# Performance work log

Hardware: AMD Instinct MI355X
Metric: run time of the kernel (lower is better)

Reference implementation:

```python
import jax, jax.numpy as jnp
import numpy as np

B, S, HN, TN = 8, 32, 64, 512
HID, EMB, VOCAB = 512, 512, 10000


def setup_inputs():
    key = jax.random.key(0)
    k = jax.random.split(key, 14)
    w = lambda kk, shape: jax.random.normal(kk, shape, jnp.float32) * 0.02
    return {
        "dec_out": jax.random.normal(k[0], (B, S, HID), jnp.float32),
        "history": jax.random.normal(k[1], (B, HID), jnp.float32),
        "head": jax.random.randint(k[2], (B, HN), 0, VOCAB),
        "tail": jax.random.randint(k[3], (B, TN), 0, VOCAB),
        "adj_mask": jax.random.randint(k[4], (B, HN, TN), 0, 2).astype(bool),
        "dup_mask": jax.random.randint(k[5], (B, S, TN), 0, 2).astype(bool),
        "emb_table": w(k[6], (VOCAB, EMB)),
        "W_tq": w(k[7], (2 * HID + EMB, HID)),
        "b_tq": jnp.zeros((HID,), jnp.float32),
        "W_tk": w(k[8], (EMB, HID)),
        "b_tk": jnp.zeros((HID,), jnp.float32),
        "W_tout": w(k[9], (2 * HID, HID)),
        "W_hq": w(k[10], (2 * HID, HID)),
        "b_hq": jnp.zeros((HID,), jnp.float32),
        "W_hk": w(k[11], (HID, HID)),
        "b_hk": jnp.zeros((HID,), jnp.float32),
    }


def reference(dec_out, history, head, tail, adj_mask, dup_mask, emb_table,
              W_tq, b_tq, W_tk, b_tk, W_tout, W_hq, b_hq, W_hk, b_hk):
    head_emb = emb_table[head]  # (B, HN, EMB)
    tail_emb = emb_table[tail]  # (B, TN, EMB)

    # --- tail attention query: Linear(cat([dec_out, history, head_emb])) + ELU.
    # Same math as the torch broadcast-concat, computed as a sum of three
    # partial matmuls to avoid materializing the (B,S,HN,2*hid+emb) concat.
    Wd, Wh, We = W_tq[:HID], W_tq[HID:2 * HID], W_tq[2 * HID:]
    tq = jax.nn.elu((dec_out @ Wd)[:, :, None, :]
                    + (history @ Wh)[:, None, None, :]
                    + (head_emb @ We)[:, None, :, :]
                    + b_tq)                       # (B, S, HN, HID)
    tq = tq.reshape(B, S * HN, HID)
    tk = jax.nn.elu(tail_emb @ W_tk + b_tk)       # (B, TN, HID)  (dropout=eval)

    # combined logical mask: allowed = adjacency AND not-duplicate
    mask = (adj_mask[:, None, :, :] & ~dup_mask[:, :, None, :]).reshape(B, S * HN, TN)

    # GlobalAttention (dot): score -> mask -> softmax -> context -> tanh(linear_out([c;q]))
    scores = jnp.einsum('bqh,bth->bqt', tq, tk)   # (B, S*HN, TN)
    tail_attn = jax.nn.softmax(jnp.where(mask, scores, -jnp.inf), axis=-1)
    ctx = jnp.einsum('bqt,bth->bqh', tail_attn, tk)
    graph_hid = jnp.tanh(ctx @ W_tout[:HID] + tq @ W_tout[HID:])
    graph_hid = graph_hid.reshape(B * S, HN, HID)
    tail_attn = tail_attn.reshape(B * S, HN, TN)

    # --- head attention (one-step), length-masked over HN
    hq = jax.nn.elu(dec_out @ W_hq[:HID] + (history @ W_hq[HID:])[:, None, :] + b_hq)
    hq = hq.reshape(B * S, HID)
    hk = jax.nn.elu(jnp.einsum('nkh,hd->nkd', graph_hid, W_hk) + b_hk)
    lengths = jnp.repeat(jnp.sum(head != 0, axis=-1), S)          # (B*S,)
    hscores = jnp.einsum('nh,nkh->nk', hq, hk)                    # (B*S, HN)
    lmask = jnp.arange(HN)[None, :] < lengths[:, None]
    head_attn = jax.nn.softmax(jnp.where(lmask, hscores, -jnp.inf), axis=-1)
    # (head-attention context output is discarded by the original module)

    prob = jnp.einsum('nk,nkt->nt', head_attn, tail_attn).reshape(B, S, TN)
    return jnp.log(prob + 1e-20)
```

## Files before the change

kernel.cpp:

```cpp
#include <hip/hip_runtime.h>
#include <math.h>

#define BB 8
#define SS 32
#define HN 64
#define TN 512
#define HID 512

typedef __attribute__((ext_vector_type(8))) short short8;
typedef __attribute__((ext_vector_type(4))) float f32x4;

__device__ __forceinline__ float eluf(float x) { return x > 0.f ? x : (expf(x) - 1.f); }

__device__ __forceinline__ short f2bs(float f) {
    union { float f; unsigned int u; } v; v.f = f;
    unsigned int r = v.u + 0x7fffu + ((v.u >> 16) & 1u);
    return (short)(r >> 16);
}
__device__ __forceinline__ float b2f(short s) {
    union { unsigned int u; float f; } v;
    v.u = ((unsigned int)(unsigned short)s) << 16;
    return v.f;
}

__device__ __forceinline__ void gld16(const void* g, void* l) {
    __builtin_amdgcn_global_load_lds(
        (const __attribute__((address_space(1))) void*)g,
        (__attribute__((address_space(3))) void*)l, 16, 0, 0);
}

template <int ACT, int OUTB>
__device__ __forceinline__ void gcore(
    const short* __restrict__ A, const short* __restrict__ B,
    const float* __restrict__ bias, void* __restrict__ Cv,
    int ldc, int K, int m0, int n0, int cm0, short* Ls)
{
    short* Al = Ls;
    short* Bl = Ls + 8192;
    const int tid  = threadIdx.x;
    const int lane = tid & 63;
    const int w    = tid >> 6;
    const int wr   = w >> 1, wc = w & 1;
    const int l16  = lane & 15, quad = lane >> 4;

    const int srow = w * 16 + (lane >> 2);
    const int scol = (lane & 3) * 8;

    f32x4 acc[4][4];
#pragma unroll
    for (int i = 0; i < 4; ++i)
#pragma unroll
        for (int j = 0; j < 4; ++j) { acc[i][j][0]=0.f; acc[i][j][1]=0.f; acc[i][j][2]=0.f; acc[i][j][3]=0.f; }

    short* lA = Al + w * 512;
    short* lB = Bl + w * 512;
    const long rstep = (long)64 * K;

    const short* Ag = A + (long)(m0 + srow) * K + scol;
    const short* Bg = B + (long)(n0 + srow) * K + scol;
    for (int kt = 0; kt < K; kt += 64) {
        __syncthreads();
        gld16(Ag + kt, lA);
        gld16(Ag + kt + rstep, lA + 2048);
        gld16(Ag + kt + 32, lA + 4096);
        gld16(Ag + kt + 32 + rstep, lA + 4096 + 2048);
        gld16(Bg + kt, lB);
        gld16(Bg + kt + rstep, lB + 2048);
        gld16(Bg + kt + 32, lB + 4096);
        gld16(Bg + kt + 32 + rstep, lB + 4096 + 2048);
        __syncthreads();
#pragma unroll
        for (int h = 0; h < 2; ++h) {
            short8 af[4], bf4[4];
#pragma unroll
            for (int mi = 0; mi < 4; ++mi)
                af[mi] = *(const short8*)(Al + h * 4096 + (wr * 64 + mi * 16 + l16) * 32 + quad * 8);
#pragma unroll
            for (int ni = 0; ni < 4; ++ni)
                bf4[ni] = *(const short8*)(Bl + h * 4096 + (wc * 64 + ni * 16 + l16) * 32 + quad * 8);
#pragma unroll
            for (int mi = 0; mi < 4; ++mi)
#pragma unroll
                for (int ni = 0; ni < 4; ++ni)
                    acc[mi][ni] = __builtin_amdgcn_mfma_f32_16x16x32_bf16(af[mi], bf4[ni], acc[mi][ni], 0, 0, 0);
        }
    }

    __syncthreads();

    float bv[4];
#pragma unroll
    for (int ni = 0; ni < 4; ++ni)
        bv[ni] = bias ? bias[n0 + wc * 64 + ni * 16 + l16] : 0.f;

    if (OUTB == 1) {
        short* eb = Ls + w * 1152;
        const int er = lane >> 2;
        const int ec = (lane & 3) * 16;
#pragma unroll
        for (int mi = 0; mi < 4; ++mi) {
#pragma unroll
            for (int ni = 0; ni < 4; ++ni)
#pragma unroll
                for (int r = 0; r < 4; ++r) {
                    float x = acc[mi][ni][r] + bv[ni];
                    if (ACT == 1) x = eluf(x);
                    eb[(quad * 4 + r) * 72 + ni * 16 + l16] = f2bs(x);
                }
            __builtin_amdgcn_sched_barrier(0);
            short8 v0 = *(const short8*)&eb[er * 72 + ec];
            short8 v1 = *(const short8*)&eb[er * 72 + ec + 8];
            long cb = (long)(cm0 + wr * 64 + mi * 16 + er) * ldc + n0 + wc * 64 + ec;
            *(short8*)((short*)Cv + cb)     = v0;
            *(short8*)((short*)Cv + cb + 8) = v1;
            __builtin_amdgcn_sched_barrier(0);
        }
    } else {
#pragma unroll
        for (int mi = 0; mi < 4; ++mi)
#pragma unroll
            for (int ni = 0; ni < 4; ++ni) {
                int gc = n0 + wc * 64 + ni * 16 + l16;
#pragma unroll
                for (int r = 0; r < 4; ++r) {
                    float x = acc[mi][ni][r] + bv[ni];
                    if (ACT == 1) x = eluf(x);
                    ((float*)Cv)[(long)(cm0 + wr * 64 + mi * 16 + quad * 4 + r) * ldc + gc] = x;
                }
            }
    }
}

template <int ACT, int OUTB, int DUAL>
__device__ __forceinline__ void gcoreB(
    const short* __restrict__ A, const short* __restrict__ B,
    const short* __restrict__ A2, const short* __restrict__ B2,
    const float* __restrict__ bias, void* __restrict__ Cv,
    int ldc, int K, int m0, int n0, int cm0, short* Ls,
    const float* __restrict__ hq, float* __restrict__ hsp)
{
    short* Al = Ls;
    short* Bl = Ls + 16384;
    const int tid  = threadIdx.x;
    const int lane = tid & 63;
    const int w    = tid >> 6;
    const int wr   = w >> 1, wc = w & 1;
    const int l16  = lane & 15, quad = lane >> 4;

    const int srow = w * 16 + (lane >> 2);
    const int scol = (lane & 3) * 8;

    f32x4 acc[4][4];
#pragma unroll
    for (int i = 0; i < 4; ++i)
#pragma unroll
        for (int j = 0; j < 4; ++j) { acc[i][j][0]=0.f; acc[i][j][1]=0.f; acc[i][j][2]=0.f; acc[i][j][3]=0.f; }

    short* lA = Al + w * 512;
    short* lB = Bl + w * 512;
    const long rstep = (long)64 * K;

    for (int rep = 0; rep <= DUAL; ++rep) {
        const short* Ag = (rep ? A2 : A) + (long)(m0 + srow) * K + scol;
        const short* Bg = (rep ? B2 : B) + (long)(n0 + srow) * K + scol;
        for (int kt = 0; kt < K; kt += 128) {
            __syncthreads();
#pragma unroll
            for (int h = 0; h < 4; ++h) {
                gld16(Ag + kt + h * 32,         lA + h * 4096);
                gld16(Ag + kt + h * 32 + rstep, lA + h * 4096 + 2048);
                gld16(Bg + kt + h * 32,         lB + h * 4096);
                gld16(Bg + kt + h * 32 + rstep, lB + h * 4096 + 2048);
            }
            __syncthreads();
#pragma unroll
            for (int h = 0; h < 4; ++h) {
                short8 af[4], bf4[4];
#pragma unroll
                for (int mi = 0; mi < 4; ++mi)
                    af[mi] = *(const short8*)(Al + h * 4096 + (wr * 64 + mi * 16 + l16) * 32 + quad * 8);
#pragma unroll
                for (int ni = 0; ni < 4; ++ni)
                    bf4[ni] = *(const short8*)(Bl + h * 4096 + (wc * 64 + ni * 16 + l16) * 32 + quad * 8);
#pragma unroll
                for (int mi = 0; mi < 4; ++mi)
#pragma unroll
                    for (int ni = 0; ni < 4; ++ni)
                        acc[mi][ni] = __builtin_amdgcn_mfma_f32_16x16x32_bf16(af[mi], bf4[ni], acc[mi][ni], 0, 0, 0);
            }
        }
    }

    __syncthreads();

    float bv[4];
#pragma unroll
    for (int ni = 0; ni < 4; ++ni)
        bv[ni] = bias ? bias[n0 + wc * 64 + ni * 16 + l16] : 0.f;

    if (OUTB == 1) {
        short* eb = Ls + w * 1152;
        const int er = lane >> 2;
        const int ec = (lane & 3) * 16;
#pragma unroll
        for (int mi = 0; mi < 4; ++mi) {
#pragma unroll
            for (int ni = 0; ni < 4; ++ni)
#pragma unroll
                for (int r = 0; r < 4; ++r) {
                    float x = acc[mi][ni][r] + bv[ni];
                    if (ACT == 1) x = eluf(x);
                    else if (ACT == 2) x = tanhf(x);
                    eb[(quad * 4 + r) * 72 + ni * 16 + l16] = f2bs(x);
                }
            __builtin_amdgcn_sched_barrier(0);
            short8 v0 = *(const short8*)&eb[er * 72 + ec];
            short8 v1 = *(const short8*)&eb[er * 72 + ec + 8];
            long cb = (long)(cm0 + wr * 64 + mi * 16 + er) * ldc + n0 + wc * 64 + ec;
            *(short8*)((short*)Cv + cb)     = v0;
            *(short8*)((short*)Cv + cb + 8) = v1;
            __builtin_amdgcn_sched_barrier(0);
        }
    } else if (OUTB == 2) {
        const int n_w = (cm0 + wr * 64) >> 6;
        float hqv[4];
#pragma unroll
        for (int ni = 0; ni < 4; ++ni)
            hqv[ni] = hq[(long)n_w * 512 + n0 + wc * 64 + ni * 16 + l16];
        float* red = (float*)Ls;
#pragma unroll
        for (int mi = 0; mi < 4; ++mi)
#pragma unroll
            for (int r = 0; r < 4; ++r) {
                float p = 0.f;
#pragma unroll
                for (int ni = 0; ni < 4; ++ni) {
                    float x = acc[mi][ni][r] + bv[ni];
                    if (ACT == 1) x = eluf(x);
                    p += x * hqv[ni];
                }
                p += __shfl_xor(p, 1);
                p += __shfl_xor(p, 2);
                p += __shfl_xor(p, 4);
                p += __shfl_xor(p, 8);
                if (l16 == 0) red[w * 64 + mi * 16 + quad * 4 + r] = p;
            }
        __syncthreads();
        if (tid < 128) {
            int wr2 = tid >> 6, rw = tid & 63;
            float v = red[(wr2 * 2 + 0) * 64 + rw] + red[(wr2 * 2 + 1) * 64 + rw];
            hsp[(long)(n0 >> 7) * 16384 + cm0 + tid] = v;
        }
    }
}

template <int ACT, int OUTB, int DUAL, int NYL2>
__global__ __launch_bounds__(256) void mgemm_sw(
    const short* __restrict__ A, long sAz,
    const short* __restrict__ B, long sBz,
    const short* __restrict__ A2, long sA2z,
    const short* __restrict__ B2,
    const float* __restrict__ bias,
    void* __restrict__ Cv, long sCz, int ldc, int K)
{
    __shared__ short Ls[32768];
    const int bid = blockIdx.x;
    const int g = (bid & 7) + 8 * (bid >> 5);
    const int x = (bid >> 3) & 3;
    const int y = g & ((1 << NYL2) - 1);
    const int z = g >> NYL2;
    void* C = (void*)((short*)Cv + (long)z * sCz);
    const short* A2z = DUAL ? (A2 + (long)z * sA2z) : nullptr;
    gcoreB<ACT, OUTB, DUAL>(A + (long)z * sAz, B + (long)z * sBz, A2z, B2, bias, C,
                            ldc, K, y * 128, x * 128, y * 128, Ls, nullptr, nullptr);
}

__global__ __launch_bounds__(256) void mgemm_hs(
    const short* __restrict__ A, const short* __restrict__ B,
    const float* __restrict__ bias, const float* __restrict__ hq, float* __restrict__ hsp)
{
    __shared__ short Ls[32768];
    const int bid = blockIdx.x;
    const int y = (bid & 7) + 8 * (bid >> 5);
    const int x = (bid >> 3) & 3;
    gcoreB<1, 2, 0>(A, B, nullptr, nullptr, bias, nullptr, 512, 512,
                    y * 128, x * 128, y * 128, Ls, hq, hsp);
}

__global__ __launch_bounds__(256) void mgemm_multi(
    const short* __restrict__ decb, const short* __restrict__ WTall, float* __restrict__ qall,
    const short* __restrict__ embAll, const short* __restrict__ WTe, float* __restrict__ qe,
    const short* __restrict__ WTk, const float* __restrict__ b_tk, short* __restrict__ tkb)
{
    __shared__ short Ls[16384];
    int id = blockIdx.x;
    if (id < 48) {
        int y = id >> 4, x = id & 15;
        gcore<0, 0>(decb, WTall, nullptr, qall, 2048, 512, y * 128, x * 128, y * 128, Ls);
    } else if (id < 64) {
        int id2 = id - 48, y = id2 >> 2, x = id2 & 3;
        gcore<0, 0>(embAll, WTe, nullptr, qe, 512, 512, y * 128, x * 128, y * 128, Ls);
    } else {
        int id3 = id - 64, y = id3 >> 2, x = id3 & 3;
        gcore<1, 1>(embAll, WTk, b_tk, tkb, 512, 512, 512 + y * 128, x * 128, y * 128, Ls);
    }
}

struct WTDesc { const float* src[9]; short* dst[9]; };

__global__ __launch_bounds__(256) void prep(
    const float* __restrict__ dec_out, const float* __restrict__ history,
    short* __restrict__ decb,
    const float* __restrict__ emb, const int* __restrict__ head, const int* __restrict__ tail,
    short* __restrict__ embAll, WTDesc wd)
{
    __shared__ float t[32][33];
    const int id = blockIdx.x, tid = threadIdx.x;
    if (id < 132) {
        int i = (id * 256 + tid) * 4;
        float4 v = (i < 131072) ? *(const float4*)(dec_out + i)
                                : *(const float4*)(history + (i - 131072));
        short4 o;
        o.x = f2bs(v.x); o.y = f2bs(v.y); o.z = f2bs(v.z); o.w = f2bs(v.w);
        *(short4*)(decb + i) = o;
    } else if (id < 132 + 2304) {
        int r = (id - 132) * 2 + (tid >> 7);
        int c4 = (tid & 127) * 4;
        int idx = (r < 512) ? head[r] : tail[r - 512];
        float4 v = *(const float4*)(emb + (long)idx * 512 + c4);
        short4 o;
        o.x = f2bs(v.x); o.y = f2bs(v.y); o.z = f2bs(v.z); o.w = f2bs(v.w);
        *(short4*)(embAll + (long)r * 512 + c4) = o;
    } else {
        int q = id - 2436;
        int z = q >> 8, xy = q & 255;
        int x = xy & 15, y = xy >> 4;
        const float* src = wd.src[z];
        short* dst = wd.dst[z];
        int k0 = y * 32, n0 = x * 32;
        int tx = tid & 31, ty = tid >> 5;
#pragma unroll
        for (int i = 0; i < 32; i += 8)
            t[ty + i][tx] = src[(long)(k0 + ty + i) * 512 + n0 + tx];
        __syncthreads();
#pragma unroll
        for (int i = 0; i < 32; i += 8)
            dst[(long)(n0 + ty + i) * 512 + k0 + tx] = f2bs(t[tx][ty + i]);
    }
}

__global__ __launch_bounds__(256) void l3_kernel(
    const float* __restrict__ qall, const float* __restrict__ qe,
    const float* __restrict__ b_tq, short* __restrict__ tqb,
    const short* __restrict__ WTo1, const short* __restrict__ tkb, short* __restrict__ tkWTb,
    const float* __restrict__ b_hq, float* __restrict__ hqf)
{
    __shared__ short Ls[16384];
    if (blockIdx.x < 8192) {
        long gid = (long)blockIdx.x * 256 + threadIdx.x;
        int r = (int)(gid >> 7), j0 = ((int)gid & 127) * 4;
        int b = r >> 11, rem = r & 2047, s = rem >> 6, h = rem & 63;
        float4 d = *(const float4*)(qall + (long)(b * 32 + s) * 2048 + j0);
        float4 q = *(const float4*)(qall + (long)(256 + b) * 2048 + 1024 + j0);
        float4 e = *(const float4*)(qe + (long)(b * 64 + h) * 512 + j0);
        float4 bb = *(const float4*)(b_tq + j0);
        short4 o;
        o.x = f2bs(eluf(d.x + q.x + e.x + bb.x));
        o.y = f2bs(eluf(d.y + q.y + e.y + bb.y));
        o.z = f2bs(eluf(d.z + q.z + e.z + bb.z));
        o.w = f2bs(eluf(d.w + q.w + e.w + bb.w));
        *(short4*)(tqb + (long)r * 512 + j0) = o;
    } else if (blockIdx.x < 8320) {
        int id2 = blockIdx.x - 8192;
        int z = id2 >> 4, r = id2 & 15;
        int x = r & 3, y = r >> 2;
        gcore<0, 1>(WTo1, tkb + (long)z * 262144, nullptr,
                    tkWTb + (long)z * 262144, 512, 512, y * 128, x * 128, y * 128, Ls);
    } else {
        long gid = (long)(blockIdx.x - 8320) * 256 + threadIdx.x;
        int n = (int)(gid >> 7), j0 = ((int)gid & 127) * 4;
        int b = n >> 5;
        float4 d = *(const float4*)(qall + (long)n * 2048 + 512 + j0);
        float4 h2 = *(const float4*)(qall + (long)(256 + b) * 2048 + 1536 + j0);
        float4 bb = *(const float4*)(b_hq + j0);
        float4 o;
        o.x = eluf(d.x + h2.x + bb.x);
        o.y = eluf(d.y + h2.y + bb.y);
        o.z = eluf(d.z + h2.z + bb.z);
        o.w = eluf(d.w + h2.w + bb.w);
        *(float4*)(hqf + (long)n * 512 + j0) = o;
    }
}

__global__ __launch_bounds__(256) void sm_kernel(
    const short* __restrict__ sc, const int* __restrict__ adj, const int* __restrict__ dup,
    short* __restrict__ Pb)
{
    int w = threadIdx.x >> 6, lane = threadIdx.x & 63;
    long r = (long)blockIdx.x * 4 + w;
    int b = (int)(r >> 11), rem = (int)(r & 2047), s = rem >> 6, h = rem & 63;
    const short* row = sc + r * 512 + lane * 8;
    const int* adjr = adj + ((long)(b * 64 + h)) * 512 + lane * 8;
    const int* dupr = dup + ((long)(b * 32 + s)) * 512 + lane * 8;
    short8 v8 = *(const short8*)row;
    int4 a0 = *(const int4*)adjr, a1 = *(const int4*)(adjr + 4);
    int4 d0 = *(const int4*)dupr, d1 = *(const int4*)(dupr + 4);
    int am[8] = {a0.x, a0.y, a0.z, a0.w, a1.x, a1.y, a1.z, a1.w};
    int dm[8] = {d0.x, d0.y, d0.z, d0.w, d1.x, d1.y, d1.z, d1.w};
    float v[8];
    float m = -INFINITY;
#pragma unroll
    for (int i = 0; i < 8; ++i) {
        v[i] = (am[i] && !dm[i]) ? b2f(v8[i]) : -INFINITY;
        m = fmaxf(m, v[i]);
    }
#pragma unroll
    for (int d = 32; d >= 1; d >>= 1) m = fmaxf(m, __shfl_xor(m, d));
    float sum = 0.f;
#pragma unroll
    for (int i = 0; i < 8; ++i) {
        float e = (m == -INFINITY) ? 0.f : expf(v[i] - m);
        v[i] = e; sum += e;
    }
#pragma unroll
    for (int d = 32; d >= 1; d >>= 1) sum += __shfl_xor(sum, d);
    float inv = sum > 0.f ? 1.f / sum : 0.f;
    short8 o;
#pragma unroll
    for (int i = 0; i < 8; ++i) o[i] = f2bs(v[i] * inv);
    *(short8*)(Pb + r * 512 + lane * 8) = o;
}

__global__ __launch_bounds__(256) void fused_head(
    const float* __restrict__ hsp, const int* __restrict__ head,
    const short* __restrict__ ta, float* __restrict__ out)
{
    int n = blockIdx.x, b = n >> 5;
    int tid = threadIdx.x;
    __shared__ float hal[64];
    __shared__ float part[4][512];

    if (tid < 64) {
        float sv_raw = hsp[n * 64 + tid] + hsp[16384 + n * 64 + tid]
                     + hsp[2 * 16384 + n * 64 + tid] + hsp[3 * 16384 + n * 64 + tid];
        int hv = head[b * 64 + tid];
        unsigned long long ball = __ballot(hv != 0);
        int len = __popcll(ball);
        float sv = (tid < len) ? sv_raw : -INFINITY;
        float m = sv;
#pragma unroll
        for (int d = 32; d >= 1; d >>= 1) m = fmaxf(m, __shfl_xor(m, d));
        float e = expf(sv - m);
        float sum = e;
#pragma unroll
        for (int d = 32; d >= 1; d >>= 1) sum += __shfl_xor(sum, d);
        hal[tid] = e / sum;
    }
    __syncthreads();

    {
        int w = tid >> 6, lane = tid & 63;
        const short* tab = ta + (long)n * 64 * 512 + (long)(w * 16) * 512 + lane * 8;
        float acc[8] = {};
#pragma unroll
        for (int k = 0; k < 16; ++k) {
            float a = hal[w * 16 + k];
            short8 tv = *(const short8*)(tab + (long)k * 512);
#pragma unroll
            for (int u = 0; u < 8; ++u) acc[u] += a * b2f(tv[u]);
        }
        float4* pp = (float4*)&part[w][lane * 8];
        pp[0] = make_float4(acc[0], acc[1], acc[2], acc[3]);
        pp[1] = make_float4(acc[4], acc[5], acc[6], acc[7]);
    }
    __syncthreads();

    for (int t = tid; t < 512; t += 256) {
        float a = part[0][t] + part[1][t] + part[2][t] + part[3][t];
        out[(long)n * 512 + t] = logf(a + 1e-20f);
    }
}

extern "C" void kernel_launch(void* const* d_in, const int* in_sizes, int n_in,
                              void* d_out, int out_size, void* d_ws, size_t ws_size,
                              hipStream_t stream)
{
    const float* dec_out = (const float*)d_in[0];
    const float* history = (const float*)d_in[1];
    const int*   head    = (const int*)d_in[2];
    const int*   tail    = (const int*)d_in[3];
    const int*   adj     = (const int*)d_in[4];
    const int*   dup     = (const int*)d_in[5];
    const float* emb     = (const float*)d_in[6];
    const float* W_tq    = (const float*)d_in[7];
    const float* b_tq    = (const float*)d_in[8];
    const float* W_tk    = (const float*)d_in[9];
    const float* b_tk    = (const float*)d_in[10];
    const float* W_tout  = (const float*)d_in[11];
    const float* W_hq    = (const float*)d_in[12];
    const float* b_hq    = (const float*)d_in[13];
    const float* W_hk    = (const float*)d_in[14];
    const float* b_hk    = (const float*)d_in[15];
    float* out = (float*)d_out;

    char* ws = (char*)d_ws;
    auto alloc = [&](size_t bytes) -> void* {
        char* p = ws;
        ws += (bytes + 255) & ~(size_t)255;
        return (void*)p;
    };
    short* decb   = (short*)alloc((size_t)384 * 512 * 2);
    short* embAll = (short*)alloc((size_t)4608 * 512 * 2);
    short* WT     = (short*)alloc((size_t)9 * 512 * 512 * 2);
    float* qall   = (float*)alloc((size_t)384 * 2048 * 4);
    float* qe     = (float*)alloc((size_t)512 * 512 * 4);
    float* hqf    = (float*)alloc((size_t)256 * 512 * 4);
    float* hsp    = (float*)alloc((size_t)4 * 16384 * 4);
    short* tkb    = (short*)alloc((size_t)4096 * 512 * 2);
    short* tkWTb  = (short*)alloc((size_t)4096 * 512 * 2);
    short* tqb    = (short*)alloc((size_t)16384 * 512 * 2);
    short* scb    = (short*)alloc((size_t)16384 * 512 * 2);
    short* Pb     = (short*)alloc((size_t)16384 * 512 * 2);
    short* ghb = scb;

    WTDesc wd;
    wd.src[0] = W_tq;               wd.dst[0] = WT;
    wd.src[1] = W_hq;               wd.dst[1] = WT + (size_t)1 * 262144;
    wd.src[2] = W_tq + 512 * 512;   wd.dst[2] = WT + (size_t)2 * 262144;
    wd.src[3] = W_hq + 512 * 512;   wd.dst[3] = WT + (size_t)3 * 262144;
    wd.src[4] = W_tq + 1024 * 512;  wd.dst[4] = WT + (size_t)4 * 262144;
    wd.src[5] = W_tk;               wd.dst[5] = WT + (size_t)5 * 262144;
    wd.src[6] = W_tout;             wd.dst[6] = WT + (size_t)6 * 262144;
    wd.src[7] = W_tout + 512 * 512; wd.dst[7] = WT + (size_t)7 * 262144;
    wd.src[8] = W_hk;               wd.dst[8] = WT + (size_t)8 * 262144;

    prep<<<4740, 256, 0, stream>>>(dec_out, history, decb, emb, head, tail, embAll, wd);
    mgemm_multi<<<192, 256, 0, stream>>>(decb, WT, qall, embAll, WT + (size_t)4 * 262144, qe,
                                         WT + (size_t)5 * 262144, b_tk, tkb);
    l3_kernel<<<8448, 256, 0, stream>>>(qall, qe, b_tq, tqb, WT + (size_t)6 * 262144, tkb, tkWTb,
                                        b_hq, hqf);
    mgemm_sw<0, 1, 0, 4><<<512, 256, 0, stream>>>(
        tqb, (long)2048 * 512, tkb, 262144, nullptr, 0, nullptr, nullptr,
        scb, (long)2048 * 512, 512, 512);
    sm_kernel<<<4096, 256, 0, stream>>>(scb, adj, dup, Pb);
    mgemm_sw<2, 1, 1, 4><<<512, 256, 0, stream>>>(
        Pb, (long)2048 * 512, tkWTb, 262144, tqb, (long)2048 * 512, WT + (size_t)7 * 262144,
        nullptr, ghb, (long)2048 * 512, 512, 512);
    mgemm_hs<<<512, 256, 0, stream>>>(ghb, WT + (size_t)8 * 262144, b_hk, hqf, hsp);
    fused_head<<<256, 256, 0, stream>>>(hsp, head, Pb, out);
}
```

Before: 211.3 us.

## Run score and head-key GEMMs in FP8 with fp8 MFMA

Adds a software float-to-FP8 (e4m3) converter and produces FP8 copies of tq, tk, graph_hid and W_hk. The score GEMM (tq·tk) and the head-key GEMM now use fp8 MFMA instructions with 256-wide K tiles, and the graph_hid output is written directly as FP8. The goal is to halve operand bytes and use the higher fp8 MFMA throughput on the two large GEMMs. The cost is extra conversion work in l3_kernel and the epilogues, plus a precision loss on scores that feed the softmax, which may exceed tolerance.

```diff
diff --git a/kernel.cpp b/kernel.cpp
--- a/kernel.cpp
+++ b/kernel.cpp
@@ -21,6 +21,24 @@
     union { unsigned int u; float f; } v;
     v.u = ((unsigned int)(unsigned short)s) << 16;
     return v.f;
+}
+
+__device__ __forceinline__ unsigned char f2f8(float x) {
+    union { float f; unsigned u; } v; v.f = x;
+    unsigned s = (v.u >> 24) & 0x80;
+    unsigned au = v.u & 0x7fffffffu;
+    if (au >= 0x43e80000u) return (unsigned char)(s | 0x7e);
+    if (au < 0x3c800000u) {
+        union { unsigned u; float f; } a; a.u = au;
+        int q = (int)rintf(a.f * 512.f);
+        return (unsigned char)(s | (unsigned)q);
+    }
+    unsigned r = au + 0x7ffffu + ((au >> 20) & 1u);
+    unsigned e = (r >> 23) - 120u;
+    unsigned m = (r >> 20) & 7u;
+    unsigned out = (e << 3) | m;
+    if (out > 0x7eu) out = 0x7eu;
+    return (unsigned char)(s | out);
 }
 
 __device__ __forceinline__ void gld16(const void* g, void* l) {
@@ -131,13 +149,11 @@
     }
 }
 
-template <int ACT, int OUTB, int DUAL>
-__device__ __forceinline__ void gcoreB(
+__device__ __forceinline__ void gcore_gh(
     const short* __restrict__ A, const short* __restrict__ B,
     const short* __restrict__ A2, const short* __restrict__ B2,
-    const float* __restrict__ bias, void* __restrict__ Cv,
-    int ldc, int K, int m0, int n0, int cm0, short* Ls,
-    const float* __restrict__ hq, float* __restrict__ hsp)
+    unsigned char* __restrict__ C8,
+    int m0, int n0, int cm0, short* Ls)
 {
     short* Al = Ls;
     short* Bl = Ls + 16384;
@@ -158,12 +174,12 @@
 
     short* lA = Al + w * 512;
     short* lB = Bl + w * 512;
-    const long rstep = (long)64 * K;
-
-    for (int rep = 0; rep <= DUAL; ++rep) {
-        const short* Ag = (rep ? A2 : A) + (long)(m0 + srow) * K + scol;
-        const short* Bg = (rep ? B2 : B) + (long)(n0 + srow) * K + scol;
-        for (int kt = 0; kt < K; kt += 128) {
+    const long rstep = (long)64 * 512;
+
+    for (int rep = 0; rep <= 1; ++rep) {
+        const short* Ag = (rep ? A2 : A) + (long)(m0 + srow) * 512 + scol;
+        const short* Bg = (rep ? B2 : B) + (long)(n0 + srow) * 512 + scol;
+        for (int kt = 0; kt < 512; kt += 128) {
             __syncthreads();
 #pragma unroll
             for (int h = 0; h < 4; ++h) {
@@ -193,13 +209,86 @@
 
     __syncthreads();
 
+    unsigned char* eb = (unsigned char*)Ls + w * 1280;
+    const int er = lane >> 2;
+    const int ec = (lane & 3) * 16;
+#pragma unroll
+    for (int mi = 0; mi < 4; ++mi) {
+#pragma unroll
+        for (int ni = 0; ni < 4; ++ni)
+#pragma unroll
+            for (int r = 0; r < 4; ++r)
+                eb[(quad * 4 + r) * 80 + ni * 16 + l16] = f2f8(tanhf(acc[mi][ni][r]));
+        __builtin_amdgcn_sched_barrier(0);
+        int4 v = *(const int4*)(eb + er * 80 + ec);
+        *(int4*)(C8 + (long)(cm0 + wr * 64 + mi * 16 + er) * 512 + n0 + wc * 64 + ec) = v;
+        __builtin_amdgcn_sched_barrier(0);
+    }
+}
+
+template <int OUTB>
+__device__ __forceinline__ void gcoreF(
+    const unsigned char* __restrict__ A, const unsigned char* __restrict__ B,
+    const float* __restrict__ bias, void* __restrict__ Cv,
+    int ldc, int m0, int n0, int cm0, unsigned char* Ls,
+    const float* __restrict__ hq, float* __restrict__ hsp)
+{
+    unsigned char* Al = Ls;
+    unsigned char* Bl = Ls + 32768;
+    const int tid  = threadIdx.x;
+    const int lane = tid & 63;
+    const int w    = tid >> 6;
+    const int wr   = w >> 1, wc = w & 1;
+    const int l16  = lane & 15, quad = lane >> 4;
+
+    const int srow = w * 32 + (lane >> 1);
+    const int scol = (lane & 1) * 16;
+
+    f32x4 acc[4][4];
+#pragma unroll
+    for (int i = 0; i < 4; ++i)
+#pragma unroll
+        for (int j = 0; j < 4; ++j) { acc[i][j][0]=0.f; acc[i][j][1]=0.f; acc[i][j][2]=0.f; acc[i][j][3]=0.f; }
+
+    const unsigned char* Ag = A + (long)(m0 + srow) * 512 + scol;
+    const unsigned char* Bg = B + (long)(n0 + srow) * 512 + scol;
+    unsigned char* lA = Al + w * 1024;
+    unsigned char* lB = Bl + w * 1024;
+
+    for (int kt = 0; kt < 512; kt += 256) {
+        __syncthreads();
+#pragma unroll
+        for (int h = 0; h < 8; ++h) {
+            gld16(Ag + kt + h * 32, lA + h * 4096);
+            gld16(Bg + kt + h * 32, lB + h * 4096);
+        }
+        __syncthreads();
+#pragma unroll
+        for (int h = 0; h < 8; ++h) {
+            long af[4], bf4[4];
+#pragma unroll
+            for (int mi = 0; mi < 4; ++mi)
+                af[mi] = *(const long*)(Al + h * 4096 + (wr * 64 + mi * 16 + l16) * 32 + quad * 8);
+#pragma unroll
+            for (int ni = 0; ni < 4; ++ni)
+                bf4[ni] = *(const long*)(Bl + h * 4096 + (wc * 64 + ni * 16 + l16) * 32 + quad * 8);
+#pragma unroll
+            for (int mi = 0; mi < 4; ++mi)
+#pragma unroll
+                for (int ni = 0; ni < 4; ++ni)
+                    acc[mi][ni] = __builtin_amdgcn_mfma_f32_16x16x32_fp8_fp8(af[mi], bf4[ni], acc[mi][ni], 0, 0, 0);
+        }
+    }
+
+    __syncthreads();
+
     float bv[4];
 #pragma unroll
     for (int ni = 0; ni < 4; ++ni)
         bv[ni] = bias ? bias[n0 + wc * 64 + ni * 16 + l16] : 0.f;
 
     if (OUTB == 1) {
-        short* eb = Ls + w * 1152;
+        short* eb = (short*)Ls + w * 1152;
         const int er = lane >> 2;
         const int ec = (lane & 3) * 16;
 #pragma unroll
@@ -207,12 +296,8 @@
 #pragma unroll
             for (int ni = 0; ni < 4; ++ni)
 #pragma unroll
-                for (int r = 0; r < 4; ++r) {
-                    float x = acc[mi][ni][r] + bv[ni];
-                    if (ACT == 1) x = eluf(x);
-                    else if (ACT == 2) x = tanhf(x);
-                    eb[(quad * 4 + r) * 72 + ni * 16 + l16] = f2bs(x);
-                }
+                for (int r = 0; r < 4; ++r)
+                    eb[(quad * 4 + r) * 72 + ni * 16 + l16] = f2bs(acc[mi][ni][r] + bv[ni]);
             __builtin_amdgcn_sched_barrier(0);
             short8 v0 = *(const short8*)&eb[er * 72 + ec];
             short8 v1 = *(const short8*)&eb[er * 72 + ec + 8];
@@ -221,7 +306,7 @@
             *(short8*)((short*)Cv + cb + 8) = v1;
             __builtin_amdgcn_sched_barrier(0);
         }
-    } else if (OUTB == 2) {
+    } else {
         const int n_w = (cm0 + wr * 64) >> 6;
         float hqv[4];
 #pragma unroll
@@ -234,11 +319,8 @@
             for (int r = 0; r < 4; ++r) {
                 float p = 0.f;
 #pragma unroll
-                for (int ni = 0; ni < 4; ++ni) {
-                    float x = acc[mi][ni][r] + bv[ni];
-                    if (ACT == 1) x = eluf(x);
-                    p += x * hqv[ni];
-                }
+                for (int ni = 0; ni < 4; ++ni)
+                    p += eluf(acc[mi][ni][r] + bv[ni]) * hqv[ni];
                 p += __shfl_xor(p, 1);
                 p += __shfl_xor(p, 2);
                 p += __shfl_xor(p, 4);
@@ -254,37 +336,46 @@
     }
 }
 
-template <int ACT, int OUTB, int DUAL, int NYL2>
-__global__ __launch_bounds__(256) void mgemm_sw(
-    const short* __restrict__ A, long sAz,
-    const short* __restrict__ B, long sBz,
-    const short* __restrict__ A2, long sA2z,
-    const short* __restrict__ B2,
-    const float* __restrict__ bias,
-    void* __restrict__ Cv, long sCz, int ldc, int K)
+__global__ __launch_bounds__(256) void mgemm_f8(
+    const unsigned char* __restrict__ A, const unsigned char* __restrict__ B,
+    short* __restrict__ Cb)
+{
+    __shared__ unsigned char Ls[65536];
+    const int bid = blockIdx.x;
+    const int g = (bid & 7) + 8 * (bid >> 5);
+    const int x = (bid >> 3) & 3;
+    const int y = g & 15;
+    const int z = g >> 4;
+    gcoreF<1>(A + (long)z * 2048 * 512, B + (long)z * 262144, nullptr,
+              Cb + (long)z * 2048 * 512, 512, y * 128, x * 128, y * 128, Ls,
+              nullptr, nullptr);
+}
+
+__global__ __launch_bounds__(256) void mgemm_hs8(
+    const unsigned char* __restrict__ A, const unsigned char* __restrict__ B,
+    const float* __restrict__ bias, const float* __restrict__ hq, float* __restrict__ hsp)
+{
+    __shared__ unsigned char Ls[65536];
+    const int bid = blockIdx.x;
+    const int y = (bid & 7) + 8 * (bid >> 5);
+    const int x = (bid >> 3) & 3;
+    gcoreF<2>(A, B, bias, nullptr, 512, y * 128, x * 128, y * 128, Ls, hq, hsp);
+}
+
+__global__ __launch_bounds__(256) void mgemm_gh(
+    const short* __restrict__ Pb, const short* __restrict__ tkWTb,
+    const short* __restrict__ tqb, const short* __restrict__ WTo2,
+    unsigned char* __restrict__ gh8)
 {
     __shared__ short Ls[32768];
     const int bid = blockIdx.x;
     const int g = (bid & 7) + 8 * (bid >> 5);
     const int x = (bid >> 3) & 3;
-    const int y = g & ((1 << NYL2) - 1);
-    const int z = g >> NYL2;
-    void* C = (void*)((short*)Cv + (long)z * sCz);
-    const short* A2z = DUAL ? (A2 + (long)z * sA2z) : nullptr;
-    gcoreB<ACT, OUTB, DUAL>(A + (long)z * sAz, B + (long)z * sBz, A2z, B2, bias, C,
-                            ldc, K, y * 128, x * 128, y * 128, Ls, nullptr, nullptr);
-}
-
-__global__ __launch_bounds__(256) void mgemm_hs(
-    const short* __restrict__ A, const short* __restrict__ B,
-    const float* __restrict__ bias, const float* __restrict__ hq, float* __restrict__ hsp)
-{
-    __shared__ short Ls[32768];
-    const int bid = blockIdx.x;
-    const int y = (bid & 7) + 8 * (bid >> 5);
-    const int x = (bid >> 3) & 3;
-    gcoreB<1, 2, 0>(A, B, nullptr, nullptr, bias, nullptr, 512, 512,
-                    y * 128, x * 128, y * 128, Ls, hq, hsp);
+    const int y = g & 15;
+    const int z = g >> 4;
+    gcore_gh(Pb + (long)z * 2048 * 512, tkWTb + (long)z * 262144,
+             tqb + (long)z * 2048 * 512, WTo2,
+             gh8 + (long)z * 2048 * 512, y * 128, x * 128, y * 128, Ls);
 }
 
 __global__ __launch_bounds__(256) void mgemm_multi(
@@ -336,24 +427,31 @@
         int z = q >> 8, xy = q & 255;
         int x = xy & 15, y = xy >> 4;
         const float* src = wd.src[z];
-        short* dst = wd.dst[z];
         int k0 = y * 32, n0 = x * 32;
         int tx = tid & 31, ty = tid >> 5;
 #pragma unroll
         for (int i = 0; i < 32; i += 8)
             t[ty + i][tx] = src[(long)(k0 + ty + i) * 512 + n0 + tx];
         __syncthreads();
-#pragma unroll
-        for (int i = 0; i < 32; i += 8)
-            dst[(long)(n0 + ty + i) * 512 + k0 + tx] = f2bs(t[tx][ty + i]);
+        if (z == 8) {
+            unsigned char* d8 = (unsigned char*)wd.dst[z];
+#pragma unroll
+            for (int i = 0; i < 32; i += 8)
+                d8[(long)(n0 + ty + i) * 512 + k0 + tx] = f2f8(t[tx][ty + i]);
+        } else {
+            short* dst = wd.dst[z];
+#pragma unroll
+            for (int i = 0; i < 32; i += 8)
+                dst[(long)(n0 + ty + i) * 512 + k0 + tx] = f2bs(t[tx][ty + i]);
+        }
     }
 }
 
 __global__ __launch_bounds__(256) void l3_kernel(
     const float* __restrict__ qall, const float* __restrict__ qe,
-    const float* __restrict__ b_tq, short* __restrict__ tqb,
+    const float* __restrict__ b_tq, short* __restrict__ tqb, unsigned char* __restrict__ tq8,
     const short* __restrict__ WTo1, const short* __restrict__ tkb, short* __restrict__ tkWTb,
-    const float* __restrict__ b_hq, float* __restrict__ hqf)
+    const float* __restrict__ b_hq, float* __restrict__ hqf, unsigned char* __restrict__ tk8)
 {
     __shared__ short Ls[16384];
     if (blockIdx.x < 8192) {
@@ -364,19 +462,23 @@
         float4 q = *(const float4*)(qall + (long)(256 + b) * 2048 + 1024 + j0);
         float4 e = *(const float4*)(qe + (long)(b * 64 + h) * 512 + j0);
         float4 bb = *(const float4*)(b_tq + j0);
+        float f0 = eluf(d.x + q.x + e.x + bb.x);
+        float f1 = eluf(d.y + q.y + e.y + bb.y);
+        float f2 = eluf(d.z + q.z + e.z + bb.z);
+        float f3 = eluf(d.w + q.w + e.w + bb.w);
         short4 o;
-        o.x = f2bs(eluf(d.x + q.x + e.x + bb.x));
-        o.y = f2bs(eluf(d.y + q.y + e.y + bb.y));
-        o.z = f2bs(eluf(d.z + q.z + e.z + bb.z));
-        o.w = f2bs(eluf(d.w + q.w + e.w + bb.w));
+        o.x = f2bs(f0); o.y = f2bs(f1); o.z = f2bs(f2); o.w = f2bs(f3);
         *(short4*)(tqb + (long)r * 512 + j0) = o;
+        uchar4 o8;
+        o8.x = f2f8(f0); o8.y = f2f8(f1); o8.z = f2f8(f2); o8.w = f2f8(f3);
+        *(uchar4*)(tq8 + (long)r * 512 + j0) = o8;
     } else if (blockIdx.x < 8320) {
         int id2 = blockIdx.x - 8192;
         int z = id2 >> 4, r = id2 & 15;
         int x = r & 3, y = r >> 2;
         gcore<0, 1>(WTo1, tkb + (long)z * 262144, nullptr,
                     tkWTb + (long)z * 262144, 512, 512, y * 128, x * 128, y * 128, Ls);
-    } else {
+    } else if (blockIdx.x < 8448) {
         long gid = (long)(blockIdx.x - 8320) * 256 + threadIdx.x;
         int n = (int)(gid >> 7), j0 = ((int)gid & 127) * 4;
         int b = n >> 5;
@@ -389,6 +491,19 @@
         o.z = eluf(d.z + h2.z + bb.z);
         o.w = eluf(d.w + h2.w + bb.w);
         *(float4*)(hqf + (long)n * 512 + j0) = o;
+    } else {
+        long base = ((long)(blockIdx.x - 8448) * 256 + threadIdx.x) * 16;
+        short8 a0 = *(const short8*)(tkb + base);
+        short8 a1 = *(const short8*)(tkb + base + 8);
+        unsigned int p[4];
+#pragma unroll
+        for (int j = 0; j < 2; ++j) {
+            p[j] = (unsigned)f2f8(b2f(a0[j*4+0])) | ((unsigned)f2f8(b2f(a0[j*4+1])) << 8)
+                 | ((unsigned)f2f8(b2f(a0[j*4+2])) << 16) | ((unsigned)f2f8(b2f(a0[j*4+3])) << 24);
+            p[2+j] = (unsigned)f2f8(b2f(a1[j*4+0])) | ((unsigned)f2f8(b2f(a1[j*4+1])) << 8)
+                 | ((unsigned)f2f8(b2f(a1[j*4+2])) << 16) | ((unsigned)f2f8(b2f(a1[j*4+3])) << 24);
+        }
+        *(uint4*)(tk8 + base) = make_uint4(p[0], p[1], p[2], p[3]);
     }
 }
 
@@ -521,7 +636,9 @@
     short* tqb    = (short*)alloc((size_t)16384 * 512 * 2);
     short* scb    = (short*)alloc((size_t)16384 * 512 * 2);
     short* Pb     = (short*)alloc((size_t)16384 * 512 * 2);
-    short* ghb = scb;
+    unsigned char* tq8 = (unsigned char*)alloc((size_t)16384 * 512);
+    unsigned char* tk8 = (unsigned char*)alloc((size_t)4096 * 512);
+    unsigned char* gh8 = (unsigned char*)scb;
 
     WTDesc wd;
     wd.src[0] = W_tq;               wd.dst[0] = WT;
@@ -537,15 +654,12 @@
     prep<<<4740, 256, 0, stream>>>(dec_out, history, decb, emb, head, tail, embAll, wd);
     mgemm_multi<<<192, 256, 0, stream>>>(decb, WT, qall, embAll, WT + (size_t)4 * 262144, qe,
                                          WT + (size_t)5 * 262144, b_tk, tkb);
-    l3_kernel<<<8448, 256, 0, stream>>>(qall, qe, b_tq, tqb, WT + (size_t)6 * 262144, tkb, tkWTb,
-                                        b_hq, hqf);
-    mgemm_sw<0, 1, 0, 4><<<512, 256, 0, stream>>>(
-        tqb, (long)2048 * 512, tkb, 262144, nullptr, 0, nullptr, nullptr,
-        scb, (long)2048 * 512, 512, 512);
+    l3_kernel<<<8960, 256, 0, stream>>>(qall, qe, b_tq, tqb, tq8, WT + (size_t)6 * 262144,
+                                        tkb, tkWTb, b_hq, hqf, tk8);
+    mgemm_f8<<<512, 256, 0, stream>>>(tq8, tk8, scb);
     sm_kernel<<<4096, 256, 0, stream>>>(scb, adj, dup, Pb);
-    mgemm_sw<2, 1, 1, 4><<<512, 256, 0, stream>>>(
-        Pb, (long)2048 * 512, tkWTb, 262144, tqb, (long)2048 * 512, WT + (size_t)7 * 262144,
-        nullptr, ghb, (long)2048 * 512, 512, 512);
-    mgemm_hs<<<512, 256, 0, stream>>>(ghb, WT + (size_t)8 * 262144, b_hk, hqf, hsp);
+    mgemm_gh<<<512, 256, 0, stream>>>(Pb, tkWTb, tqb, WT + (size_t)7 * 262144, gh8);
+    mgemm_hs8<<<512, 256, 0, stream>>>(gh8, (const unsigned char*)(WT + (size_t)8 * 262144),
+                                       b_hk, hqf, hsp);
     fused_head<<<256, 256, 0, stream>>>(hsp, head, Pb, out);
 }
```

Measured after the change: 223.3 us. 5.6% more time.
